# Performance work log

Measured on AMD Instinct MI355X. Metric: run time of the kernel, lower is better.

Reference implementation:

```python
import jax, jax.numpy as jnp
import numpy as np

NUM_STEPS = 100
ALPHA = 0.9      # learn_alpha=False default in snn.Synaptic
THRESHOLD = 1.0
SLOPE = 25.0     # fast_sigmoid default slope

@jax.custom_vjp
def spike_fn(x):
    # Heaviside forward with fast-sigmoid surrogate gradient
    return (x > 0).astype(x.dtype)

def _spike_fwd(x):
    return (x > 0).astype(x.dtype), x

def _spike_bwd(x, g):
    return (g / (SLOPE * jnp.abs(x) + 1.0) ** 2,)

spike_fn.defvjp(_spike_fwd, _spike_bwd)


def setup_inputs() -> dict:
    key = jax.random.key(0)
    k0, k1, k2 = jax.random.split(key, 3)
    B, NI, NH, NO = 4096, 256, 2048, 128
    x = jax.random.normal(k0, (B, NI), dtype=jnp.float32)
    # Linear init scale ~ 1/sqrt(fan_in)
    W1 = jax.random.normal(k1, (NH, NI), dtype=jnp.float32) / np.sqrt(NI)
    b1 = jnp.zeros((NH,), dtype=jnp.float32)
    W2 = jax.random.normal(k2, (NO, NH), dtype=jnp.float32) / np.sqrt(NH)
    b2 = jnp.zeros((NO,), dtype=jnp.float32)
    beta = jnp.asarray(0.85, dtype=jnp.float32)  # learnable scalar
    return {"x": x, "W1": W1, "b1": b1, "W2": W2, "b2": b2, "beta": beta}


def reference(x, W1, b1, W2, b2, beta):
    # cur1 = fc1(x) is identical every step -> hoist (same math)
    cur1 = x @ W1.T + b1                      # [B, NH]
    beta_c = jnp.clip(beta, 0.0, 1.0)
    B, NH = cur1.shape
    z = jnp.zeros((B, NH), dtype=cur1.dtype)

    def step(carry, _):
        syn, mem, _spk = carry
        # reset-by-subtraction from detached pre-update membrane
        reset = jax.lax.stop_gradient((mem > THRESHOLD).astype(mem.dtype))
        syn = ALPHA * syn + cur1
        mem = beta_c * mem + syn - reset * THRESHOLD
        spk = spike_fn(mem - THRESHOLD)
        return (syn, mem, spk), None

    (syn, mem, spk), _ = jax.lax.scan(step, (z, z, z), None, length=NUM_STEPS)
    cur2 = spk @ W2.T + b2                    # [B, NO]
    return cur2
```

## Files before the change

### kernel.cpp

```cpp
#include <hip/hip_runtime.h>
#include <stdint.h>


typedef __attribute__((ext_vector_type(8))) short short8;
typedef __attribute__((ext_vector_type(4))) float floatx4;

#define NSTEPS 100

static __device__ __forceinline__ uint32_t f2bf2(float lo, float hi) {
  union { float f; uint32_t u; } a, b; a.f = lo; b.f = hi;
  uint32_t x = (a.u + 0x7FFFu + ((a.u >> 16) & 1u)) >> 16;
  uint32_t y = (b.u + 0x7FFFu + ((b.u >> 16) & 1u)) & 0xFFFF0000u;
  return x | y;
}

__global__ __launch_bounds__(256, 4) void snn_k1(
    const float* __restrict__ X, const float* __restrict__ W1,
    const float* __restrict__ b1, const float* __restrict__ betap,
    uint16_t* __restrict__ spk)
{
  __shared__ __align__(16) float As[32 * 68];
  __shared__ __align__(16) float Bs[32 * 68];
  const int tid = threadIdx.x;
  const int bm  = blockIdx.y * 64;
  const int bn  = blockIdx.x * 64;
  const int ty  = tid >> 4;
  const int tx  = tid & 15;
  const int sc  = tid & 7;
  const int sr  = tid >> 3;

  float acc[4][4] = {};

  float4 xa[2], wa[2];
  #pragma unroll
  for (int h = 0; h < 2; ++h) {
    const int r = sr + h * 32;
    xa[h] = *(const float4*)(X  + (size_t)(bm + r) * 256 + sc * 4);
    wa[h] = *(const float4*)(W1 + (size_t)(bn + r) * 256 + sc * 4);
  }

  #pragma unroll 1
  for (int k0 = 0; k0 < 256; k0 += 32) {
    #pragma unroll
    for (int h = 0; h < 2; ++h) {
      const int r = sr + h * 32;
      As[(sc * 4 + 0) * 68 + r] = xa[h].x;
      As[(sc * 4 + 1) * 68 + r] = xa[h].y;
      As[(sc * 4 + 2) * 68 + r] = xa[h].z;
      As[(sc * 4 + 3) * 68 + r] = xa[h].w;
      Bs[(sc * 4 + 0) * 68 + r] = wa[h].x;
      Bs[(sc * 4 + 1) * 68 + r] = wa[h].y;
      Bs[(sc * 4 + 2) * 68 + r] = wa[h].z;
      Bs[(sc * 4 + 3) * 68 + r] = wa[h].w;
    }
    __syncthreads();

    if (k0 < 224) {
      const int kn = k0 + 32;
      #pragma unroll
      for (int h = 0; h < 2; ++h) {
        const int r = sr + h * 32;
        xa[h] = *(const float4*)(X  + (size_t)(bm + r) * 256 + kn + sc * 4);
        wa[h] = *(const float4*)(W1 + (size_t)(bn + r) * 256 + kn + sc * 4);
      }
    }

    #pragma unroll
    for (int kk = 0; kk < 32; ++kk) {
      const float4 a4 = *(const float4*)(As + kk * 68 + ty * 4);
      const float4 b4 = *(const float4*)(Bs + kk * 68 + tx * 4);
      const float av[4] = {a4.x, a4.y, a4.z, a4.w};
      const float bv[4] = {b4.x, b4.y, b4.z, b4.w};
      #pragma unroll
      for (int i = 0; i < 4; ++i)
        #pragma unroll
        for (int j = 0; j < 4; ++j)
          acc[i][j] += av[i] * bv[j];
    }
    __syncthreads();
  }

  float beta = betap[0];
  beta = fminf(fmaxf(beta, 0.0f), 1.0f);
  float bias[4];
  #pragma unroll
  for (int j = 0; j < 4; ++j) bias[j] = b1[bn + tx * 4 + j];

  float cc[16];
  #pragma unroll
  for (int i = 0; i < 4; ++i)
    #pragma unroll
    for (int j = 0; j < 4; ++j)
      cc[i * 4 + j] = acc[i][j] + bias[j];

  #pragma unroll
  for (int h = 0; h < 2; ++h) {
    float syn[8], mem[8];
    #pragma unroll
    for (int e = 0; e < 8; ++e) { syn[e] = 0.0f; mem[e] = 0.0f; }

    #pragma unroll 1
    for (int t = 0; t < NSTEPS; ++t) {
      #pragma unroll
      for (int e = 0; e < 8; ++e) {
        const float rst = (mem[e] > 1.0f) ? 1.0f : 0.0f;
        syn[e] = __fadd_rn(__fmul_rn(0.9f, syn[e]), cc[h * 8 + e]);
        mem[e] = __fsub_rn(__fadd_rn(__fmul_rn(beta, mem[e]), syn[e]), rst);
      }
    }

    #pragma unroll
    for (int i = 0; i < 2; ++i) {
      ushort4 o;
      o.x = (mem[i * 4 + 0] > 1.0f) ? (uint16_t)0x3F80u : (uint16_t)0u;
      o.y = (mem[i * 4 + 1] > 1.0f) ? (uint16_t)0x3F80u : (uint16_t)0u;
      o.z = (mem[i * 4 + 2] > 1.0f) ? (uint16_t)0x3F80u : (uint16_t)0u;
      o.w = (mem[i * 4 + 3] > 1.0f) ? (uint16_t)0x3F80u : (uint16_t)0u;
      *(ushort4*)(spk + (size_t)(bm + ty * 4 + h * 2 + i) * 2048 + bn + tx * 4) = o;
    }
  }
}

#define PS 72

__global__ __launch_bounds__(256) void snn_k2(
    const uint16_t* __restrict__ spk, const float* __restrict__ W2,
    float* __restrict__ part)
{
  __shared__ short As[128 * PS];
  __shared__ short Bs[128 * PS];
  const int tid  = threadIdx.x;
  const int lane = tid & 63;
  const int w    = tid >> 6;
  const int wm   = (w >> 1) * 64;
  const int wn   = (w & 1) * 64;
  const int bm   = blockIdx.x * 128;
  const int kc   = blockIdx.y;

  floatx4 acc[4][4] = {};

  #pragma unroll 1
  for (int kk = 0; kk < 4; ++kk) {
    const int k0 = kc * 256 + kk * 64;
    #pragma unroll
    for (int p = 0; p < 4; ++p) {
      const int u = p * 256 + tid;
      const int r = u >> 3, c = u & 7;
      const int4 va = *(const int4*)(spk + (size_t)(bm + r) * 2048 + k0 + c * 8);
      *(int4*)(As + r * PS + c * 8) = va;
    }
    #pragma unroll
    for (int p = 0; p < 4; ++p) {
      const int u = p * 256 + tid;
      const int n = u >> 3, c = u & 7;
      const float* wp = W2 + (size_t)n * 2048 + k0 + c * 8;
      const float4 w0 = *(const float4*)(wp);
      const float4 w1 = *(const float4*)(wp + 4);
      int4 pk;
      pk.x = (int)f2bf2(w0.x, w0.y);
      pk.y = (int)f2bf2(w0.z, w0.w);
      pk.z = (int)f2bf2(w1.x, w1.y);
      pk.w = (int)f2bf2(w1.z, w1.w);
      *(int4*)(Bs + n * PS + c * 8) = pk;
    }
    __syncthreads();

    #pragma unroll
    for (int ks = 0; ks < 2; ++ks) {
      const int kb = ks * 4 + (lane >> 4);
      const int fe = lane & 15;
      short8 a8[4], b8[4];
      #pragma unroll
      for (int tm = 0; tm < 4; ++tm)
        a8[tm] = *(const short8*)(As + (wm + tm * 16 + fe) * PS + kb * 8);
      #pragma unroll
      for (int tn = 0; tn < 4; ++tn)
        b8[tn] = *(const short8*)(Bs + (wn + tn * 16 + fe) * PS + kb * 8);
      #pragma unroll
      for (int tm = 0; tm < 4; ++tm)
        #pragma unroll
        for (int tn = 0; tn < 4; ++tn)
          acc[tm][tn] = __builtin_amdgcn_mfma_f32_16x16x32_bf16(
              a8[tm], b8[tn], acc[tm][tn], 0, 0, 0);
    }
    __syncthreads();
  }

  const int fe = lane & 15;
  const int fr = (lane >> 4) * 4;
  #pragma unroll
  for (int tm = 0; tm < 4; ++tm)
    #pragma unroll
    for (int tn = 0; tn < 4; ++tn)
      #pragma unroll
      for (int r = 0; r < 4; ++r) {
        const int row = bm + wm + tm * 16 + fr + r;
        const int col = wn + tn * 16 + fe;
        part[((size_t)kc * 4096 + row) * 128 + col] = acc[tm][tn][r];
      }
}

__global__ __launch_bounds__(256) void snn_k3(
    const float* __restrict__ part, const float* __restrict__ b2,
    float* __restrict__ out)
{
  const int idx = blockIdx.x * 256 + threadIdx.x;
  const int m = idx >> 5;
  const int c = (idx & 31) << 2;
  float s0 = 0.f, s1 = 0.f, s2 = 0.f, s3 = 0.f;
  #pragma unroll
  for (int kc = 0; kc < 8; ++kc) {
    const float4 p = *(const float4*)(part + ((size_t)kc * 4096 + m) * 128 + c);
    s0 += p.x; s1 += p.y; s2 += p.z; s3 += p.w;
  }
  float4 o;
  o.x = s0 + b2[c + 0];
  o.y = s1 + b2[c + 1];
  o.z = s2 + b2[c + 2];
  o.w = s3 + b2[c + 3];
  *(float4*)(out + (size_t)m * 128 + c) = o;
}

extern "C" void kernel_launch(void* const* d_in, const int* in_sizes, int n_in,
                              void* d_out, int out_size, void* d_ws, size_t ws_size,
                              hipStream_t stream) {
  const float* X    = (const float*)d_in[0];
  const float* W1   = (const float*)d_in[1];
  const float* b1   = (const float*)d_in[2];
  const float* W2   = (const float*)d_in[3];
  const float* b2   = (const float*)d_in[4];
  const float* beta = (const float*)d_in[5];
  float* out = (float*)d_out;

  uint16_t* spk = (uint16_t*)d_ws;
  float* part = (float*)((char*)d_ws + (size_t)4096 * 2048 * 2);

  snn_k1<<<dim3(32, 64), 256, 0, stream>>>(X, W1, b1, beta, spk);
  snn_k2<<<dim3(32, 8), 256, 0, stream>>>(spk, W2, part);
  snn_k3<<<512, 256, 0, stream>>>(part, b2, out);
}
```

Baseline: 215.0 us.

## Enlarge fc1 tile to 128x128 with 8x8 per-thread micro-tile

```diff
diff --git a/kernel.cpp b/kernel.cpp
--- a/kernel.cpp
+++ b/kernel.cpp
@@ -19,62 +19,47 @@
     const float* __restrict__ b1, const float* __restrict__ betap,
     uint16_t* __restrict__ spk)
 {
-  __shared__ __align__(16) float As[32 * 68];
-  __shared__ __align__(16) float Bs[32 * 68];
+  __shared__ __align__(16) float As[32 * 132];
+  __shared__ __align__(16) float Bs[32 * 132];
   const int tid = threadIdx.x;
-  const int bm  = blockIdx.y * 64;
-  const int bn  = blockIdx.x * 64;
+  const int bm  = blockIdx.y * 128;
+  const int bn  = blockIdx.x * 128;
   const int ty  = tid >> 4;
   const int tx  = tid & 15;
   const int sc  = tid & 7;
   const int sr  = tid >> 3;
 
-  float acc[4][4] = {};
-
-  float4 xa[2], wa[2];
-  #pragma unroll
-  for (int h = 0; h < 2; ++h) {
-    const int r = sr + h * 32;
-    xa[h] = *(const float4*)(X  + (size_t)(bm + r) * 256 + sc * 4);
-    wa[h] = *(const float4*)(W1 + (size_t)(bn + r) * 256 + sc * 4);
-  }
+  float acc[8][8] = {};
 
   #pragma unroll 1
   for (int k0 = 0; k0 < 256; k0 += 32) {
     #pragma unroll
-    for (int h = 0; h < 2; ++h) {
-      const int r = sr + h * 32;
-      As[(sc * 4 + 0) * 68 + r] = xa[h].x;
-      As[(sc * 4 + 1) * 68 + r] = xa[h].y;
-      As[(sc * 4 + 2) * 68 + r] = xa[h].z;
-      As[(sc * 4 + 3) * 68 + r] = xa[h].w;
-      Bs[(sc * 4 + 0) * 68 + r] = wa[h].x;
-      Bs[(sc * 4 + 1) * 68 + r] = wa[h].y;
-      Bs[(sc * 4 + 2) * 68 + r] = wa[h].z;
-      Bs[(sc * 4 + 3) * 68 + r] = wa[h].w;
-    }
-    __syncthreads();
-
-    if (k0 < 224) {
-      const int kn = k0 + 32;
-      #pragma unroll
-      for (int h = 0; h < 2; ++h) {
-        const int r = sr + h * 32;
-        xa[h] = *(const float4*)(X  + (size_t)(bm + r) * 256 + kn + sc * 4);
-        wa[h] = *(const float4*)(W1 + (size_t)(bn + r) * 256 + kn + sc * 4);
-      }
-    }
-
+    for (int p = 0; p < 4; ++p) {
+      const int r = p * 32 + sr;
+      const float4 xa = *(const float4*)(X  + (size_t)(bm + r) * 256 + k0 + sc * 4);
+      const float4 wa = *(const float4*)(W1 + (size_t)(bn + r) * 256 + k0 + sc * 4);
+      As[(sc * 4 + 0) * 132 + r] = xa.x;
+      As[(sc * 4 + 1) * 132 + r] = xa.y;
+      As[(sc * 4 + 2) * 132 + r] = xa.z;
+      As[(sc * 4 + 3) * 132 + r] = xa.w;
+      Bs[(sc * 4 + 0) * 132 + r] = wa.x;
+      Bs[(sc * 4 + 1) * 132 + r] = wa.y;
+      Bs[(sc * 4 + 2) * 132 + r] = wa.z;
+      Bs[(sc * 4 + 3) * 132 + r] = wa.w;
+    }
+    __syncthreads();
     #pragma unroll
     for (int kk = 0; kk < 32; ++kk) {
-      const float4 a4 = *(const float4*)(As + kk * 68 + ty * 4);
-      const float4 b4 = *(const float4*)(Bs + kk * 68 + tx * 4);
-      const float av[4] = {a4.x, a4.y, a4.z, a4.w};
-      const float bv[4] = {b4.x, b4.y, b4.z, b4.w};
-      #pragma unroll
-      for (int i = 0; i < 4; ++i)
+      const float4 al = *(const float4*)(As + kk * 132 + ty * 4);
+      const float4 ah = *(const float4*)(As + kk * 132 + 64 + ty * 4);
+      const float4 bl = *(const float4*)(Bs + kk * 132 + tx * 4);
+      const float4 bh = *(const float4*)(Bs + kk * 132 + 64 + tx * 4);
+      const float av[8] = {al.x, al.y, al.z, al.w, ah.x, ah.y, ah.z, ah.w};
+      const float bv[8] = {bl.x, bl.y, bl.z, bl.w, bh.x, bh.y, bh.z, bh.w};
+      #pragma unroll
+      for (int i = 0; i < 8; ++i)
         #pragma unroll
-        for (int j = 0; j < 4; ++j)
+        for (int j = 0; j < 8; ++j)
           acc[i][j] += av[i] * bv[j];
     }
     __syncthreads();
@@ -82,19 +67,22 @@
 
   float beta = betap[0];
   beta = fminf(fmaxf(beta, 0.0f), 1.0f);
-  float bias[4];
-  #pragma unroll
-  for (int j = 0; j < 4; ++j) bias[j] = b1[bn + tx * 4 + j];
-
-  float cc[16];
-  #pragma unroll
-  for (int i = 0; i < 4; ++i)
-    #pragma unroll
-    for (int j = 0; j < 4; ++j)
-      cc[i * 4 + j] = acc[i][j] + bias[j];
-
-  #pragma unroll
-  for (int h = 0; h < 2; ++h) {
+  float bias[8];
+  #pragma unroll
+  for (int j = 0; j < 4; ++j) {
+    bias[j]     = b1[bn + tx * 4 + j];
+    bias[4 + j] = b1[bn + 64 + tx * 4 + j];
+  }
+
+  float cc[64];
+  #pragma unroll
+  for (int i = 0; i < 8; ++i)
+    #pragma unroll
+    for (int j = 0; j < 8; ++j)
+      cc[i * 8 + j] = acc[i][j] + bias[j];
+
+  #pragma unroll
+  for (int p = 0; p < 8; ++p) {
     float syn[8], mem[8];
     #pragma unroll
     for (int e = 0; e < 8; ++e) { syn[e] = 0.0f; mem[e] = 0.0f; }
@@ -104,20 +92,23 @@
       #pragma unroll
       for (int e = 0; e < 8; ++e) {
         const float rst = (mem[e] > 1.0f) ? 1.0f : 0.0f;
-        syn[e] = __fadd_rn(__fmul_rn(0.9f, syn[e]), cc[h * 8 + e]);
+        syn[e] = __fadd_rn(__fmul_rn(0.9f, syn[e]), cc[p * 8 + e]);
         mem[e] = __fsub_rn(__fadd_rn(__fmul_rn(beta, mem[e]), syn[e]), rst);
       }
     }
 
-    #pragma unroll
-    for (int i = 0; i < 2; ++i) {
-      ushort4 o;
-      o.x = (mem[i * 4 + 0] > 1.0f) ? (uint16_t)0x3F80u : (uint16_t)0u;
-      o.y = (mem[i * 4 + 1] > 1.0f) ? (uint16_t)0x3F80u : (uint16_t)0u;
-      o.z = (mem[i * 4 + 2] > 1.0f) ? (uint16_t)0x3F80u : (uint16_t)0u;
-      o.w = (mem[i * 4 + 3] > 1.0f) ? (uint16_t)0x3F80u : (uint16_t)0u;
-      *(ushort4*)(spk + (size_t)(bm + ty * 4 + h * 2 + i) * 2048 + bn + tx * 4) = o;
-    }
+    const int row = bm + ((p < 4) ? (ty * 4 + p) : (64 + ty * 4 + (p - 4)));
+    ushort4 olo, ohi;
+    olo.x = (mem[0] > 1.0f) ? (uint16_t)0x3F80u : (uint16_t)0u;
+    olo.y = (mem[1] > 1.0f) ? (uint16_t)0x3F80u : (uint16_t)0u;
+    olo.z = (mem[2] > 1.0f) ? (uint16_t)0x3F80u : (uint16_t)0u;
+    olo.w = (mem[3] > 1.0f) ? (uint16_t)0x3F80u : (uint16_t)0u;
+    ohi.x = (mem[4] > 1.0f) ? (uint16_t)0x3F80u : (uint16_t)0u;
+    ohi.y = (mem[5] > 1.0f) ? (uint16_t)0x3F80u : (uint16_t)0u;
+    ohi.z = (mem[6] > 1.0f) ? (uint16_t)0x3F80u : (uint16_t)0u;
+    ohi.w = (mem[7] > 1.0f) ? (uint16_t)0x3F80u : (uint16_t)0u;
+    *(ushort4*)(spk + (size_t)row * 2048 + bn + tx * 4)      = olo;
+    *(ushort4*)(spk + (size_t)row * 2048 + bn + 64 + tx * 4) = ohi;
   }
 }
 
@@ -235,7 +226,7 @@
   uint16_t* spk = (uint16_t*)d_ws;
   float* part = (float*)((char*)d_ws + (size_t)4096 * 2048 * 2);
 
-  snn_k1<<<dim3(32, 64), 256, 0, stream>>>(X, W1, b1, beta, spk);
+  snn_k1<<<dim3(16, 32), 256, 0, stream>>>(X, W1, b1, beta, spk);
   snn_k2<<<dim3(32, 8), 256, 0, stream>>>(spk, W2, part);
   snn_k3<<<512, 256, 0, stream>>>(part, b2, out);
 }
```

After: 226.9 us. 5.5% more time.

## Split GEMM1 and LIF recurrence into separate kernels, retile GEMM2 for more blocks

Applied to the files above, without the earlier changes.

```diff
diff --git a/kernel.cpp b/kernel.cpp
--- a/kernel.cpp
+++ b/kernel.cpp
@@ -14,10 +14,9 @@
   return x | y;
 }
 
-__global__ __launch_bounds__(256, 4) void snn_k1(
+__global__ __launch_bounds__(256, 4) void snn_gemm1(
     const float* __restrict__ X, const float* __restrict__ W1,
-    const float* __restrict__ b1, const float* __restrict__ betap,
-    uint16_t* __restrict__ spk)
+    const float* __restrict__ b1, float* __restrict__ cur1)
 {
   __shared__ __align__(16) float As[32 * 68];
   __shared__ __align__(16) float Bs[32 * 68];
@@ -80,70 +79,82 @@
     __syncthreads();
   }
 
+  float bias[4];
+  #pragma unroll
+  for (int j = 0; j < 4; ++j) bias[j] = b1[bn + tx * 4 + j];
+
+  #pragma unroll
+  for (int i = 0; i < 4; ++i) {
+    float4 o;
+    o.x = acc[i][0] + bias[0];
+    o.y = acc[i][1] + bias[1];
+    o.z = acc[i][2] + bias[2];
+    o.w = acc[i][3] + bias[3];
+    *(float4*)(cur1 + (size_t)(bm + ty * 4 + i) * 2048 + bn + tx * 4) = o;
+  }
+}
+
+__global__ __launch_bounds__(256) void snn_recur(
+    const float* __restrict__ cur1, const float* __restrict__ betap,
+    uint16_t* __restrict__ spk)
+{
+  const size_t base = ((size_t)blockIdx.x * 256 + threadIdx.x) * 8;
   float beta = betap[0];
   beta = fminf(fmaxf(beta, 0.0f), 1.0f);
-  float bias[4];
-  #pragma unroll
-  for (int j = 0; j < 4; ++j) bias[j] = b1[bn + tx * 4 + j];
-
-  float cc[16];
-  #pragma unroll
-  for (int i = 0; i < 4; ++i)
-    #pragma unroll
-    for (int j = 0; j < 4; ++j)
-      cc[i * 4 + j] = acc[i][j] + bias[j];
-
-  #pragma unroll
-  for (int h = 0; h < 2; ++h) {
-    float syn[8], mem[8];
-    #pragma unroll
-    for (int e = 0; e < 8; ++e) { syn[e] = 0.0f; mem[e] = 0.0f; }
-
-    #pragma unroll 1
-    for (int t = 0; t < NSTEPS; ++t) {
-      #pragma unroll
-      for (int e = 0; e < 8; ++e) {
-        const float rst = (mem[e] > 1.0f) ? 1.0f : 0.0f;
-        syn[e] = __fadd_rn(__fmul_rn(0.9f, syn[e]), cc[h * 8 + e]);
-        mem[e] = __fsub_rn(__fadd_rn(__fmul_rn(beta, mem[e]), syn[e]), rst);
-      }
-    }
-
-    #pragma unroll
-    for (int i = 0; i < 2; ++i) {
-      ushort4 o;
-      o.x = (mem[i * 4 + 0] > 1.0f) ? (uint16_t)0x3F80u : (uint16_t)0u;
-      o.y = (mem[i * 4 + 1] > 1.0f) ? (uint16_t)0x3F80u : (uint16_t)0u;
-      o.z = (mem[i * 4 + 2] > 1.0f) ? (uint16_t)0x3F80u : (uint16_t)0u;
-      o.w = (mem[i * 4 + 3] > 1.0f) ? (uint16_t)0x3F80u : (uint16_t)0u;
-      *(ushort4*)(spk + (size_t)(bm + ty * 4 + h * 2 + i) * 2048 + bn + tx * 4) = o;
-    }
-  }
+
+  const float4 c0 = *(const float4*)(cur1 + base);
+  const float4 c1 = *(const float4*)(cur1 + base + 4);
+  const float cc[8] = {c0.x, c0.y, c0.z, c0.w, c1.x, c1.y, c1.z, c1.w};
+
+  float syn[8], mem[8];
+  #pragma unroll
+  for (int e = 0; e < 8; ++e) { syn[e] = 0.0f; mem[e] = 0.0f; }
+
+  #pragma unroll 1
+  for (int t = 0; t < NSTEPS; ++t) {
+    #pragma unroll
+    for (int e = 0; e < 8; ++e) {
+      const float rst = (mem[e] > 1.0f) ? 1.0f : 0.0f;
+      syn[e] = __fadd_rn(__fmul_rn(0.9f, syn[e]), cc[e]);
+      mem[e] = __fsub_rn(__fadd_rn(__fmul_rn(beta, mem[e]), syn[e]), rst);
+    }
+  }
+
+  ushort4 olo, ohi;
+  olo.x = (mem[0] > 1.0f) ? (uint16_t)0x3F80u : (uint16_t)0u;
+  olo.y = (mem[1] > 1.0f) ? (uint16_t)0x3F80u : (uint16_t)0u;
+  olo.z = (mem[2] > 1.0f) ? (uint16_t)0x3F80u : (uint16_t)0u;
+  olo.w = (mem[3] > 1.0f) ? (uint16_t)0x3F80u : (uint16_t)0u;
+  ohi.x = (mem[4] > 1.0f) ? (uint16_t)0x3F80u : (uint16_t)0u;
+  ohi.y = (mem[5] > 1.0f) ? (uint16_t)0x3F80u : (uint16_t)0u;
+  ohi.z = (mem[6] > 1.0f) ? (uint16_t)0x3F80u : (uint16_t)0u;
+  ohi.w = (mem[7] > 1.0f) ? (uint16_t)0x3F80u : (uint16_t)0u;
+  *(ushort4*)(spk + base)     = olo;
+  *(ushort4*)(spk + base + 4) = ohi;
 }
 
 #define PS 72
 
-__global__ __launch_bounds__(256) void snn_k2(
+__global__ __launch_bounds__(256) void snn_k2m(
     const uint16_t* __restrict__ spk, const float* __restrict__ W2,
     float* __restrict__ part)
 {
-  __shared__ short As[128 * PS];
+  __shared__ short As[64 * PS];
   __shared__ short Bs[128 * PS];
   const int tid  = threadIdx.x;
   const int lane = tid & 63;
   const int w    = tid >> 6;
-  const int wm   = (w >> 1) * 64;
-  const int wn   = (w & 1) * 64;
-  const int bm   = blockIdx.x * 128;
+  const int wn   = w * 32;
+  const int bm   = blockIdx.x * 64;
   const int kc   = blockIdx.y;
 
-  floatx4 acc[4][4] = {};
-
-  #pragma unroll 1
-  for (int kk = 0; kk < 4; ++kk) {
-    const int k0 = kc * 256 + kk * 64;
-    #pragma unroll
-    for (int p = 0; p < 4; ++p) {
+  floatx4 acc[4][2] = {};
+
+  #pragma unroll 1
+  for (int kk = 0; kk < 2; ++kk) {
+    const int k0 = kc * 128 + kk * 64;
+    #pragma unroll
+    for (int p = 0; p < 2; ++p) {
       const int u = p * 256 + tid;
       const int r = u >> 3, c = u & 7;
       const int4 va = *(const int4*)(spk + (size_t)(bm + r) * 2048 + k0 + c * 8);
@@ -169,6 +180,170 @@
     for (int ks = 0; ks < 2; ++ks) {
       const int kb = ks * 4 + (lane >> 4);
       const int fe = lane & 15;
+      short8 a8[4], b8[2];
+      #pragma unroll
+      for (int tm = 0; tm < 4; ++tm)
+        a8[tm] = *(const short8*)(As + (tm * 16 + fe) * PS + kb * 8);
+      #pragma unroll
+      for (int tn = 0; tn < 2; ++tn)
+        b8[tn] = *(const short8*)(Bs + (wn + tn * 16 + fe) * PS + kb * 8);
+      #pragma unroll
+      for (int tm = 0; tm < 4; ++tm)
+        #pragma unroll
+        for (int tn = 0; tn < 2; ++tn)
+          acc[tm][tn] = __builtin_amdgcn_mfma_f32_16x16x32_bf16(
+              a8[tm], b8[tn], acc[tm][tn], 0, 0, 0);
+    }
+    __syncthreads();
+  }
+
+  const int fe = lane & 15;
+  const int fr = (lane >> 4) * 4;
+  #pragma unroll
+  for (int tm = 0; tm < 4; ++tm)
+    #pragma unroll
+    for (int tn = 0; tn < 2; ++tn)
+      #pragma unroll
+      for (int r = 0; r < 4; ++r) {
+        const int row = bm + tm * 16 + fr + r;
+        const int col = wn + tn * 16 + fe;
+        part[((size_t)kc * 4096 + row) * 128 + col] = acc[tm][tn][r];
+      }
+}
+
+__global__ __launch_bounds__(256, 4) void snn_k1_fused(
+    const float* __restrict__ X, const float* __restrict__ W1,
+    const float* __restrict__ b1, const float* __restrict__ betap,
+    uint16_t* __restrict__ spk)
+{
+  __shared__ __align__(16) float As[32 * 68];
+  __shared__ __align__(16) float Bs[32 * 68];
+  const int tid = threadIdx.x;
+  const int bm  = blockIdx.y * 64;
+  const int bn  = blockIdx.x * 64;
+  const int ty  = tid >> 4;
+  const int tx  = tid & 15;
+  const int sc  = tid & 7;
+  const int sr  = tid >> 3;
+
+  float acc[4][4] = {};
+
+  #pragma unroll 1
+  for (int k0 = 0; k0 < 256; k0 += 32) {
+    #pragma unroll
+    for (int h = 0; h < 2; ++h) {
+      const int r = sr + h * 32;
+      const float4 xa = *(const float4*)(X  + (size_t)(bm + r) * 256 + k0 + sc * 4);
+      const float4 wa = *(const float4*)(W1 + (size_t)(bn + r) * 256 + k0 + sc * 4);
+      As[(sc * 4 + 0) * 68 + r] = xa.x;
+      As[(sc * 4 + 1) * 68 + r] = xa.y;
+      As[(sc * 4 + 2) * 68 + r] = xa.z;
+      As[(sc * 4 + 3) * 68 + r] = xa.w;
+      Bs[(sc * 4 + 0) * 68 + r] = wa.x;
+      Bs[(sc * 4 + 1) * 68 + r] = wa.y;
+      Bs[(sc * 4 + 2) * 68 + r] = wa.z;
+      Bs[(sc * 4 + 3) * 68 + r] = wa.w;
+    }
+    __syncthreads();
+    #pragma unroll
+    for (int kk = 0; kk < 32; ++kk) {
+      const float4 a4 = *(const float4*)(As + kk * 68 + ty * 4);
+      const float4 b4 = *(const float4*)(Bs + kk * 68 + tx * 4);
+      const float av[4] = {a4.x, a4.y, a4.z, a4.w};
+      const float bv[4] = {b4.x, b4.y, b4.z, b4.w};
+      #pragma unroll
+      for (int i = 0; i < 4; ++i)
+        #pragma unroll
+        for (int j = 0; j < 4; ++j)
+          acc[i][j] += av[i] * bv[j];
+    }
+    __syncthreads();
+  }
+
+  float beta = betap[0];
+  beta = fminf(fmaxf(beta, 0.0f), 1.0f);
+  float bias[4];
+  #pragma unroll
+  for (int j = 0; j < 4; ++j) bias[j] = b1[bn + tx * 4 + j];
+
+  float cc[16];
+  #pragma unroll
+  for (int i = 0; i < 4; ++i)
+    #pragma unroll
+    for (int j = 0; j < 4; ++j)
+      cc[i * 4 + j] = acc[i][j] + bias[j];
+
+  #pragma unroll
+  for (int h = 0; h < 2; ++h) {
+    float syn[8], mem[8];
+    #pragma unroll
+    for (int e = 0; e < 8; ++e) { syn[e] = 0.0f; mem[e] = 0.0f; }
+    #pragma unroll 1
+    for (int t = 0; t < NSTEPS; ++t) {
+      #pragma unroll
+      for (int e = 0; e < 8; ++e) {
+        const float rst = (mem[e] > 1.0f) ? 1.0f : 0.0f;
+        syn[e] = __fadd_rn(__fmul_rn(0.9f, syn[e]), cc[h * 8 + e]);
+        mem[e] = __fsub_rn(__fadd_rn(__fmul_rn(beta, mem[e]), syn[e]), rst);
+      }
+    }
+    #pragma unroll
+    for (int i = 0; i < 2; ++i) {
+      ushort4 o;
+      o.x = (mem[i * 4 + 0] > 1.0f) ? (uint16_t)0x3F80u : (uint16_t)0u;
+      o.y = (mem[i * 4 + 1] > 1.0f) ? (uint16_t)0x3F80u : (uint16_t)0u;
+      o.z = (mem[i * 4 + 2] > 1.0f) ? (uint16_t)0x3F80u : (uint16_t)0u;
+      o.w = (mem[i * 4 + 3] > 1.0f) ? (uint16_t)0x3F80u : (uint16_t)0u;
+      *(ushort4*)(spk + (size_t)(bm + ty * 4 + h * 2 + i) * 2048 + bn + tx * 4) = o;
+    }
+  }
+}
+
+__global__ __launch_bounds__(256) void snn_k2f(
+    const uint16_t* __restrict__ spk, const float* __restrict__ W2,
+    float* __restrict__ part)
+{
+  __shared__ short As[128 * PS];
+  __shared__ short Bs[128 * PS];
+  const int tid  = threadIdx.x;
+  const int lane = tid & 63;
+  const int w    = tid >> 6;
+  const int wm   = (w >> 1) * 64;
+  const int wn   = (w & 1) * 64;
+  const int bm   = blockIdx.x * 128;
+  const int kc   = blockIdx.y;
+
+  floatx4 acc[4][4] = {};
+
+  #pragma unroll 1
+  for (int kk = 0; kk < 4; ++kk) {
+    const int k0 = kc * 256 + kk * 64;
+    #pragma unroll
+    for (int p = 0; p < 4; ++p) {
+      const int u = p * 256 + tid;
+      const int r = u >> 3, c = u & 7;
+      const int4 va = *(const int4*)(spk + (size_t)(bm + r) * 2048 + k0 + c * 8);
+      *(int4*)(As + r * PS + c * 8) = va;
+    }
+    #pragma unroll
+    for (int p = 0; p < 4; ++p) {
+      const int u = p * 256 + tid;
+      const int n = u >> 3, c = u & 7;
+      const float* wp = W2 + (size_t)n * 2048 + k0 + c * 8;
+      const float4 w0 = *(const float4*)(wp);
+      const float4 w1 = *(const float4*)(wp + 4);
+      int4 pk;
+      pk.x = (int)f2bf2(w0.x, w0.y);
+      pk.y = (int)f2bf2(w0.z, w0.w);
+      pk.z = (int)f2bf2(w1.x, w1.y);
+      pk.w = (int)f2bf2(w1.z, w1.w);
+      *(int4*)(Bs + n * PS + c * 8) = pk;
+    }
+    __syncthreads();
+    #pragma unroll
+    for (int ks = 0; ks < 2; ++ks) {
+      const int kb = ks * 4 + (lane >> 4);
+      const int fe = lane & 15;
       short8 a8[4], b8[4];
       #pragma unroll
       for (int tm = 0; tm < 4; ++tm)
@@ -202,14 +377,14 @@
 
 __global__ __launch_bounds__(256) void snn_k3(
     const float* __restrict__ part, const float* __restrict__ b2,
-    float* __restrict__ out)
+    float* __restrict__ out, int nkc)
 {
   const int idx = blockIdx.x * 256 + threadIdx.x;
   const int m = idx >> 5;
   const int c = (idx & 31) << 2;
   float s0 = 0.f, s1 = 0.f, s2 = 0.f, s3 = 0.f;
-  #pragma unroll
-  for (int kc = 0; kc < 8; ++kc) {
+  #pragma unroll 1
+  for (int kc = 0; kc < nkc; ++kc) {
     const float4 p = *(const float4*)(part + ((size_t)kc * 4096 + m) * 128 + c);
     s0 += p.x; s1 += p.y; s2 += p.z; s3 += p.w;
   }
@@ -232,10 +407,22 @@
   const float* beta = (const float*)d_in[5];
   float* out = (float*)d_out;
 
-  uint16_t* spk = (uint16_t*)d_ws;
-  float* part = (float*)((char*)d_ws + (size_t)4096 * 2048 * 2);
-
-  snn_k1<<<dim3(32, 64), 256, 0, stream>>>(X, W1, b1, beta, spk);
-  snn_k2<<<dim3(32, 8), 256, 0, stream>>>(spk, W2, part);
-  snn_k3<<<512, 256, 0, stream>>>(part, b2, out);
-}
+  const size_t CUR1_B = (size_t)4096 * 2048 * 4;
+  const size_t SPK_B  = (size_t)4096 * 2048 * 2;
+
+  if (ws_size >= CUR1_B + SPK_B) {
+    float* cur1 = (float*)d_ws;
+    uint16_t* spk = (uint16_t*)((char*)d_ws + CUR1_B);
+    float* part = (float*)d_ws;
+    snn_gemm1<<<dim3(32, 64), 256, 0, stream>>>(X, W1, b1, cur1);
+    snn_recur<<<4096, 256, 0, stream>>>(cur1, beta, spk);
+    snn_k2m<<<dim3(64, 16), 256, 0, stream>>>(spk, W2, part);
+    snn_k3<<<512, 256, 0, stream>>>(part, b2, out, 16);
+  } else {
+    uint16_t* spk = (uint16_t*)d_ws;
+    float* part = (float*)((char*)d_ws + SPK_B);
+    snn_k1_fused<<<dim3(32, 64), 256, 0, stream>>>(X, W1, b1, beta, spk);
+    snn_k2f<<<dim3(32, 8), 256, 0, stream>>>(spk, W2, part);
+    snn_k3<<<512, 256, 0, stream>>>(part, b2, out, 8);
+  }
+}
```

After: 228.3 us. +6.2%, slower.
